# Kernel optimization log

Hardware: AMD Instinct MI355X
Metric: run time of the kernel (lower is better)

The kernel has to match this reference:

```python
import jax, jax.numpy as jnp
import numpy as np

TAU = 0.11
ALPHA = 32.0  # scale
EPS = 1e-12   # torch F.normalize eps


def _l2norm(t):
    n = jnp.linalg.norm(t, axis=-1, keepdims=True)
    return t / jnp.maximum(n, EPS)


def setup_inputs() -> dict:
    key = jax.random.key(0)
    k1, k2, k3, k4 = jax.random.split(key, 4)
    B, N, C, D = 8192, 100000, 1000, 768
    return {
        "x": jax.random.normal(k1, (B, D), dtype=jnp.float32),
        "support_features": jax.random.normal(k2, (N, D), dtype=jnp.float32),
        "support_labels": jax.random.randint(k3, (N,), 0, C),
        "W": jax.random.normal(k4, (D, D), dtype=jnp.float32) * 0.02,
        "b": jnp.zeros((D,), dtype=jnp.float32),
        "num_classes": C,
    }


def reference(x, support_features, support_labels, W, b, num_classes):
    def adapter(t):
        h = t @ W.T + b              # nn.Linear(D, D)
        return jax.nn.silu(h) + t    # SiLU + residual (use_zifa)

    embeddings = _l2norm(adapter(x))                      # (B, D)
    support_key = _l2norm(adapter(support_features))      # (N, D)

    # per-class mean prototype via one segment-sum pass
    sums = jax.ops.segment_sum(support_key, support_labels, num_segments=num_classes)  # (C, D)
    counts = jax.ops.segment_sum(
        jnp.ones((support_key.shape[0],), dtype=support_key.dtype),
        support_labels, num_segments=num_classes)          # (C,)
    means = sums / jnp.maximum(counts, 1.0)[:, None]
    prototypes = jnp.where((counts > 0)[:, None], _l2norm(means), 0.0)  # (C, D)

    # mvrec logits: exp(-(alpha - alpha*cos)) / tau
    cos_sim = embeddings @ prototypes.T                    # (B, C)
    logits = jnp.exp(-(ALPHA - ALPHA * cos_sim)) / max(TAU, 1e-9)
    predicts = jax.nn.softmax(logits, axis=-1)
    return predicts, logits, embeddings
```

## Files before the change

### kernel.cpp

```cpp
#include <hip/hip_runtime.h>
#include <hip/hip_bf16.h>
#include <stdint.h>

typedef __bf16 v8bf __attribute__((ext_vector_type(8)));
typedef float  v4f  __attribute__((ext_vector_type(4)));
typedef unsigned short u16;
typedef unsigned int   u32;

#define B_ROWS   8192
#define N_SUP    100000
#define N_CLS    1000
#define DIM      768
#define CPAD     1024
#define MSUP_PAD 100352

__device__ __forceinline__ u16 f2bf(float f) {
    union { float f; u32 u; } v; v.f = f;
    u32 r = 0x7FFFu + ((v.u >> 16) & 1u);
    return (u16)((v.u + r) >> 16);
}
__device__ __forceinline__ float bf2f(u16 b) {
    union { u32 u; float f; } v; v.u = ((u32)b) << 16; return v.f;
}
__device__ __forceinline__ void glds16(const void* g, void* l) {
    __builtin_amdgcn_global_load_lds((const __attribute__((address_space(1))) u32*)g,
                                     (__attribute__((address_space(3))) u32*)l, 16, 0, 0);
}

__device__ __forceinline__ float block_sum(float v, float* red) {
    #pragma unroll
    for (int o = 32; o > 0; o >>= 1) v += __shfl_down(v, o);
    int wv = threadIdx.x >> 6, ln = threadIdx.x & 63;
    if (ln == 0) red[wv] = v;
    __syncthreads();
    return red[0] + red[1] + red[2] + red[3];
}
__device__ __forceinline__ float block_max(float v, float* red) {
    #pragma unroll
    for (int o = 32; o > 0; o >>= 1) v = fmaxf(v, __shfl_down(v, o));
    int wv = threadIdx.x >> 6, ln = threadIdx.x & 63;
    if (ln == 0) red[wv] = v;
    __syncthreads();
    return fmaxf(fmaxf(red[0], red[1]), fmaxf(red[2], red[3]));
}

__global__ void conv_pad_kernel(const float* __restrict__ in, u16* __restrict__ out,
                                int n_real) {
    int r = blockIdx.x;
    size_t ob = (size_t)r * DIM + threadIdx.x * 4;
    ushort4 o;
    if (r < n_real) {
        float4 v = *(const float4*)(in + ob);
        o.x = f2bf(v.x); o.y = f2bf(v.y); o.z = f2bf(v.z); o.w = f2bf(v.w);
    } else {
        o.x = 0; o.y = 0; o.z = 0; o.w = 0;
    }
    *(ushort4*)(out + ob) = o;
}

__global__ __launch_bounds__(256)
void adapter_gemm_kernel(const u16* __restrict__ A, const u16* __restrict__ Wb,
                         const float* __restrict__ bias,
                         u16* __restrict__ val, float* __restrict__ ss) {
    __shared__ u16 As[128 * 64];
    __shared__ u16 Bs[128 * 64];

    const int tid  = threadIdx.x;
    const int wave = tid >> 6, lane = tid & 63;
    const int fq = lane >> 4, fr = lane & 15;
    const int blk_m = blockIdx.y * 128, blk_n = blockIdx.x * 128;
    const int wm = (wave & 1) * 64, wn = (wave >> 1) * 64;

    v4f acc[4][4];
    #pragma unroll
    for (int i = 0; i < 4; i++)
        #pragma unroll
        for (int j = 0; j < 4; j++) acc[i][j] = (v4f){0.f, 0.f, 0.f, 0.f};

    const int rb = lane >> 3;
    const int cb = (lane & 7) * 8;
    const u16* gA = A  + (size_t)(blk_m + wave * 8 + rb) * DIM + cb;
    const u16* gB = Wb + (size_t)(blk_n + wave * 8 + rb) * DIM + cb;

    for (int k0 = 0; k0 < DIM; k0 += 64) {
        #pragma unroll
        for (int p = 0; p < 4; p++) {
            glds16(gA + (size_t)p * 32 * DIM + k0, As + p * 2048 + wave * 512);
            glds16(gB + (size_t)p * 32 * DIM + k0, Bs + p * 2048 + wave * 512);
        }
        __syncthreads();
        #pragma unroll
        for (int ks = 0; ks < 2; ks++) {
            const int kk = ks * 32;
            v8bf af[4], bfr[4];
            #pragma unroll
            for (int i = 0; i < 4; i++) {
                af[i]  = *(const v8bf*)(As + (wm + i * 16 + fr) * 64 + kk + fq * 8);
                bfr[i] = *(const v8bf*)(Bs + (wn + i * 16 + fr) * 64 + kk + fq * 8);
            }
            #pragma unroll
            for (int i = 0; i < 4; i++)
                #pragma unroll
                for (int j = 0; j < 4; j++)
                    acc[i][j] = __builtin_amdgcn_mfma_f32_16x16x32_bf16(
                        af[i], bfr[j], acc[i][j], 0, 0, 0);
        }
        __syncthreads();
    }

    #pragma unroll
    for (int i = 0; i < 4; i++) {
        int r0 = blk_m + wm + i * 16 + fq * 4;
        float ssp[4] = {0.f, 0.f, 0.f, 0.f};
        #pragma unroll
        for (int j = 0; j < 4; j++) {
            int col = blk_n + wn + j * 16 + fr;
            float bv = bias[col];
            #pragma unroll
            for (int r2 = 0; r2 < 4; r2++) {
                int gr = r0 + r2;
                float h = acc[i][j][r2] + bv;
                float t = bf2f(A[(size_t)gr * DIM + col]);
                float v = h / (1.f + __expf(-h)) + t;
                ssp[r2] += v * v;
                val[(size_t)gr * DIM + col] = f2bf(v);
            }
        }
        #pragma unroll
        for (int r2 = 0; r2 < 4; r2++) {
            float s = ssp[r2];
            s += __shfl_xor(s, 1); s += __shfl_xor(s, 2);
            s += __shfl_xor(s, 4); s += __shfl_xor(s, 8);
            if (fr == 0) atomicAdd(&ss[r0 + r2], s);
        }
    }
}

__global__ void norm_x_kernel(const u16* __restrict__ val, const float* __restrict__ ss,
                              float* __restrict__ emb, u16* __restrict__ emb_bf) {
    int row = blockIdx.x;
    float sc = 1.f / fmaxf(sqrtf(ss[row]), 1e-12f);
    size_t b = (size_t)row * DIM + threadIdx.x * 4;
    ushort4 v = *(const ushort4*)(val + b);
    float4 o;
    o.x = bf2f(v.x) * sc; o.y = bf2f(v.y) * sc;
    o.z = bf2f(v.z) * sc; o.w = bf2f(v.w) * sc;
    *(float4*)(emb + b) = o;
    ushort4 ob; ob.x = f2bf(o.x); ob.y = f2bf(o.y); ob.z = f2bf(o.z); ob.w = f2bf(o.w);
    *(ushort4*)(emb_bf + b) = ob;
}

__global__ __launch_bounds__(256)
void proto_kernel(const u16* __restrict__ val_bf, const float* __restrict__ ss,
                  const int* __restrict__ labels, u16* __restrict__ proto_bf) {
    __shared__ int queue[256];
    __shared__ int qn;
    __shared__ float red[4];
    const int cls = blockIdx.x, tid = threadIdx.x;
    if (tid == 0) qn = 0;
    __syncthreads();
    for (int i4 = tid; i4 < N_SUP / 4; i4 += 256) {
        int4 L = *(const int4*)(labels + i4 * 4);
        if (L.x == cls) queue[atomicAdd(&qn, 1) & 255] = i4 * 4;
        if (L.y == cls) queue[atomicAdd(&qn, 1) & 255] = i4 * 4 + 1;
        if (L.z == cls) queue[atomicAdd(&qn, 1) & 255] = i4 * 4 + 2;
        if (L.w == cls) queue[atomicAdd(&qn, 1) & 255] = i4 * 4 + 3;
    }
    __syncthreads();
    const int n = qn < 256 ? qn : 256;
    float a0 = 0.f, a1 = 0.f, a2 = 0.f;
    for (int e = 0; e < n; e++) {
        int row = queue[e];
        float sc = 1.f / fmaxf(sqrtf(ss[row]), 1e-12f);
        const u16* vr = val_bf + (size_t)row * DIM;
        a0 += bf2f(vr[tid])       * sc;
        a1 += bf2f(vr[tid + 256]) * sc;
        a2 += bf2f(vr[tid + 512]) * sc;
    }
    float inv_cnt = 1.f / fmaxf((float)n, 1.f);
    float m0 = a0 * inv_cnt, m1 = a1 * inv_cnt, m2 = a2 * inv_cnt;
    float tot = block_sum(m0 * m0 + m1 * m1 + m2 * m2, red);
    float sc2 = (n > 0) ? 1.f / fmaxf(sqrtf(tot), 1e-12f) : 0.f;
    size_t b = (size_t)cls * DIM;
    proto_bf[b + tid]       = f2bf(m0 * sc2);
    proto_bf[b + tid + 256] = f2bf(m1 * sc2);
    proto_bf[b + tid + 512] = f2bf(m2 * sc2);
}

__global__ __launch_bounds__(256)
void cos_gemm_kernel(const u16* __restrict__ Ab, const u16* __restrict__ Pb,
                     float* __restrict__ logits) {
    __shared__ u16 As[128 * 64];
    __shared__ u16 Bs[128 * 64];
    const int tid  = threadIdx.x;
    const int wave = tid >> 6, lane = tid & 63;
    const int fq = lane >> 4, fr = lane & 15;
    const int blk_m = blockIdx.y * 128, blk_n = blockIdx.x * 128;
    const int wm = (wave & 1) * 64, wn = (wave >> 1) * 64;

    v4f acc[4][4];
    #pragma unroll
    for (int i = 0; i < 4; i++)
        #pragma unroll
        for (int j = 0; j < 4; j++) acc[i][j] = (v4f){0.f, 0.f, 0.f, 0.f};

    const int rb = lane >> 3;
    const int cb = (lane & 7) * 8;
    const u16* gA = Ab + (size_t)(blk_m + wave * 8 + rb) * DIM + cb;
    const u16* gB = Pb + (size_t)(blk_n + wave * 8 + rb) * DIM + cb;

    for (int k0 = 0; k0 < DIM; k0 += 64) {
        #pragma unroll
        for (int p = 0; p < 4; p++) {
            glds16(gA + (size_t)p * 32 * DIM + k0, As + p * 2048 + wave * 512);
            glds16(gB + (size_t)p * 32 * DIM + k0, Bs + p * 2048 + wave * 512);
        }
        __syncthreads();
        #pragma unroll
        for (int ks = 0; ks < 2; ks++) {
            const int kk = ks * 32;
            v8bf af[4], bfr[4];
            #pragma unroll
            for (int i = 0; i < 4; i++) {
                af[i]  = *(const v8bf*)(As + (wm + i * 16 + fr) * 64 + kk + fq * 8);
                bfr[i] = *(const v8bf*)(Bs + (wn + i * 16 + fr) * 64 + kk + fq * 8);
            }
            #pragma unroll
            for (int i = 0; i < 4; i++)
                #pragma unroll
                for (int j = 0; j < 4; j++)
                    acc[i][j] = __builtin_amdgcn_mfma_f32_16x16x32_bf16(
                        af[i], bfr[j], acc[i][j], 0, 0, 0);
        }
        __syncthreads();
    }

    #pragma unroll
    for (int i = 0; i < 4; i++) {
        int r0 = blk_m + wm + i * 16 + fq * 4;
        #pragma unroll
        for (int j = 0; j < 4; j++) {
            int col = blk_n + wn + j * 16 + fr;
            if (col < N_CLS) {
                #pragma unroll
                for (int r2 = 0; r2 < 4; r2++) {
                    float c = acc[i][j][r2];
                    logits[(size_t)(r0 + r2) * N_CLS + col] =
                        __expf(32.0f * (c - 1.0f)) * (1.0f / 0.11f);
                }
            }
        }
    }
}

__global__ __launch_bounds__(256)
void softmax_kernel(const float* __restrict__ logits, float* __restrict__ predicts) {
    __shared__ float redm[4];
    __shared__ float reds[4];
    int row = blockIdx.x, tid = threadIdx.x;
    const float* lr = logits + (size_t)row * N_CLS;
    float4 lg = make_float4(-1.f, -1.f, -1.f, -1.f);
    bool act = tid < N_CLS / 4;
    if (act) lg = *(const float4*)(lr + tid * 4);
    float mx = fmaxf(fmaxf(lg.x, lg.y), fmaxf(lg.z, lg.w));
    float mxt = block_max(mx, redm);
    float4 e = make_float4(0.f, 0.f, 0.f, 0.f);
    float s = 0.f;
    if (act) {
        e.x = __expf(lg.x - mxt); e.y = __expf(lg.y - mxt);
        e.z = __expf(lg.z - mxt); e.w = __expf(lg.w - mxt);
        s = e.x + e.y + e.z + e.w;
    }
    float st = block_sum(s, reds);
    float inv = 1.f / st;
    if (act) {
        float4 o; o.x = e.x * inv; o.y = e.y * inv; o.z = e.z * inv; o.w = e.w * inv;
        *(float4*)(predicts + (size_t)row * N_CLS + tid * 4) = o;
    }
}

extern "C" void kernel_launch(void* const* d_in, const int* in_sizes, int n_in,
                              void* d_out, int out_size, void* d_ws, size_t ws_size,
                              hipStream_t stream) {
    const float* x      = (const float*)d_in[0];
    const float* sup    = (const float*)d_in[1];
    const int*   labels = (const int*)d_in[2];
    const float* W      = (const float*)d_in[3];
    const float* bias   = (const float*)d_in[4];

    float* predicts = (float*)d_out;
    float* logits   = predicts + (size_t)B_ROWS * N_CLS;
    float* emb      = logits + (size_t)B_ROWS * N_CLS;

    char* ws = (char*)d_ws;
    size_t off = 0;
    u16*   w_bf     = (u16*)(ws + off);   off += (size_t)DIM * DIM * 2;
    u16*   x_bf     = (u16*)(ws + off);   off += (size_t)B_ROWS * DIM * 2;
    u16*   sup_bf   = (u16*)(ws + off);   off += (size_t)MSUP_PAD * DIM * 2;
    u16*   val_x    = (u16*)(ws + off);   off += (size_t)B_ROWS * DIM * 2;
    u16*   val_sup  = (u16*)(ws + off);   off += (size_t)MSUP_PAD * DIM * 2;
    u16*   emb_bf   = (u16*)(ws + off);   off += (size_t)B_ROWS * DIM * 2;
    u16*   proto_bf = (u16*)(ws + off);   off += (size_t)CPAD * DIM * 2;
    float* ss_sup   = (float*)(ws + off); off += (size_t)MSUP_PAD * 4;
    float* ss_x     = (float*)(ws + off); off += (size_t)B_ROWS * 4;

    hipMemsetAsync(ss_sup, 0, ((size_t)MSUP_PAD + B_ROWS) * 4, stream);

    conv_pad_kernel<<<DIM,      192, 0, stream>>>(W,   w_bf,   DIM);
    conv_pad_kernel<<<B_ROWS,   192, 0, stream>>>(x,   x_bf,   B_ROWS);
    conv_pad_kernel<<<MSUP_PAD, 192, 0, stream>>>(sup, sup_bf, N_SUP);

    adapter_gemm_kernel<<<dim3(DIM / 128, B_ROWS / 128), 256, 0, stream>>>(
        x_bf, w_bf, bias, val_x, ss_x);
    adapter_gemm_kernel<<<dim3(DIM / 128, MSUP_PAD / 128), 256, 0, stream>>>(
        sup_bf, w_bf, bias, val_sup, ss_sup);

    norm_x_kernel<<<B_ROWS, 192, 0, stream>>>(val_x, ss_x, emb, emb_bf);

    proto_kernel<<<CPAD, 256, 0, stream>>>(val_sup, ss_sup, labels, proto_bf);

    cos_gemm_kernel<<<dim3(CPAD / 128, B_ROWS / 128), 256, 0, stream>>>(
        emb_bf, proto_bf, logits);
    softmax_kernel<<<B_ROWS, 256, 0, stream>>>(logits, predicts);
}
```

Baseline: 912.0 us.

## Double-buffer GEMM LDS loads, add XCD tile swizzle, widen conversion blocks

Both GEMM kernels now use two LDS buffers, so the next K-slice is loaded asynchronously while the current one feeds the MFMAs. Block IDs are remapped with an XCD-aware swizzle so neighbouring tiles run on the same XCD and share L2. The fp32-to-bf16 conversion kernel now processes four rows per 256-thread block instead of one row per 192-thread block. Costs are doubled LDS per block, which may lower occupancy, and the swizzle assumes the tile count divides evenly by 8.

Result: no change. 907.9 us (-0.4%).

```diff
diff --git a/kernel.cpp b/kernel.cpp
--- a/kernel.cpp
+++ b/kernel.cpp
@@ -10,8 +10,8 @@
 #define B_ROWS   8192
 #define N_SUP    100000
 #define N_CLS    1000
+#define CPAD     1024
 #define DIM      768
-#define CPAD     1024
 #define MSUP_PAD 100352
 
 __device__ __forceinline__ u16 f2bf(float f) {
@@ -44,31 +44,47 @@
     return fmaxf(fmaxf(red[0], red[1]), fmaxf(red[2], red[3]));
 }
 
-__global__ void conv_pad_kernel(const float* __restrict__ in, u16* __restrict__ out,
-                                int n_real) {
-    int r = blockIdx.x;
-    size_t ob = (size_t)r * DIM + threadIdx.x * 4;
-    ushort4 o;
-    if (r < n_real) {
-        float4 v = *(const float4*)(in + ob);
-        o.x = f2bf(v.x); o.y = f2bf(v.y); o.z = f2bf(v.z); o.w = f2bf(v.w);
-    } else {
-        o.x = 0; o.y = 0; o.z = 0; o.w = 0;
-    }
-    *(ushort4*)(out + ob) = o;
+__device__ __forceinline__ int xcd_swizzle(void) {
+    const int nwg = gridDim.x * gridDim.y;
+    const int bid = blockIdx.y * gridDim.x + blockIdx.x;
+    const int q = nwg >> 3;
+    return (bid & 7) * q + (bid >> 3);
+}
+
+__global__ __launch_bounds__(256)
+void conv_pad_kernel(const float* __restrict__ in, u16* __restrict__ out,
+                     int n_real) {
+    #pragma unroll
+    for (int s = 0; s < 3; s++) {
+        size_t f4 = (size_t)blockIdx.x * 768 + s * 256 + threadIdx.x;
+        int row = (int)(f4 / 192);
+        size_t eb = f4 * 4;
+        ushort4 o;
+        if (row < n_real) {
+            float4 v = *(const float4*)(in + eb);
+            o.x = f2bf(v.x); o.y = f2bf(v.y); o.z = f2bf(v.z); o.w = f2bf(v.w);
+        } else {
+            o.x = 0; o.y = 0; o.z = 0; o.w = 0;
+        }
+        *(ushort4*)(out + eb) = o;
+    }
 }
 
 __global__ __launch_bounds__(256)
 void adapter_gemm_kernel(const u16* __restrict__ A, const u16* __restrict__ Wb,
                          const float* __restrict__ bias,
                          u16* __restrict__ val, float* __restrict__ ss) {
-    __shared__ u16 As[128 * 64];
-    __shared__ u16 Bs[128 * 64];
+    __shared__ u16 As[2][128 * 64];
+    __shared__ u16 Bs[2][128 * 64];
 
     const int tid  = threadIdx.x;
     const int wave = tid >> 6, lane = tid & 63;
     const int fq = lane >> 4, fr = lane & 15;
-    const int blk_m = blockIdx.y * 128, blk_n = blockIdx.x * 128;
+
+    const int swz = xcd_swizzle();
+    const int blk_m = (swz / gridDim.x) * 128;
+    const int blk_n = (swz % gridDim.x) * 128;
+
     const int wm = (wave & 1) * 64, wn = (wave >> 1) * 64;
 
     v4f acc[4][4];
@@ -82,21 +98,22 @@
     const u16* gA = A  + (size_t)(blk_m + wave * 8 + rb) * DIM + cb;
     const u16* gB = Wb + (size_t)(blk_n + wave * 8 + rb) * DIM + cb;
 
-    for (int k0 = 0; k0 < DIM; k0 += 64) {
+    auto STAGE = [&](int buf, int k0) {
         #pragma unroll
         for (int p = 0; p < 4; p++) {
-            glds16(gA + (size_t)p * 32 * DIM + k0, As + p * 2048 + wave * 512);
-            glds16(gB + (size_t)p * 32 * DIM + k0, Bs + p * 2048 + wave * 512);
-        }
-        __syncthreads();
+            glds16(gA + (size_t)p * 32 * DIM + k0, &As[buf][p * 2048 + wave * 512]);
+            glds16(gB + (size_t)p * 32 * DIM + k0, &Bs[buf][p * 2048 + wave * 512]);
+        }
+    };
+    auto COMPUTE = [&](int buf) {
         #pragma unroll
         for (int ks = 0; ks < 2; ks++) {
             const int kk = ks * 32;
             v8bf af[4], bfr[4];
             #pragma unroll
             for (int i = 0; i < 4; i++) {
-                af[i]  = *(const v8bf*)(As + (wm + i * 16 + fr) * 64 + kk + fq * 8);
-                bfr[i] = *(const v8bf*)(Bs + (wn + i * 16 + fr) * 64 + kk + fq * 8);
+                af[i]  = *(const v8bf*)(&As[buf][(wm + i * 16 + fr) * 64 + kk + fq * 8]);
+                bfr[i] = *(const v8bf*)(&Bs[buf][(wn + i * 16 + fr) * 64 + kk + fq * 8]);
             }
             #pragma unroll
             for (int i = 0; i < 4; i++)
@@ -105,8 +122,18 @@
                     acc[i][j] = __builtin_amdgcn_mfma_f32_16x16x32_bf16(
                         af[i], bfr[j], acc[i][j], 0, 0, 0);
         }
+    };
+
+    STAGE(0, 0);
+    __syncthreads();
+    int cur = 0;
+    for (int k0 = 64; k0 < DIM; k0 += 64) {
+        STAGE(cur ^ 1, k0);
+        COMPUTE(cur);
         __syncthreads();
-    }
+        cur ^= 1;
+    }
+    COMPUTE(cur);
 
     #pragma unroll
     for (int i = 0; i < 4; i++) {
@@ -190,12 +217,16 @@
 __global__ __launch_bounds__(256)
 void cos_gemm_kernel(const u16* __restrict__ Ab, const u16* __restrict__ Pb,
                      float* __restrict__ logits) {
-    __shared__ u16 As[128 * 64];
-    __shared__ u16 Bs[128 * 64];
+    __shared__ u16 As[2][128 * 64];
+    __shared__ u16 Bs[2][128 * 64];
     const int tid  = threadIdx.x;
     const int wave = tid >> 6, lane = tid & 63;
     const int fq = lane >> 4, fr = lane & 15;
-    const int blk_m = blockIdx.y * 128, blk_n = blockIdx.x * 128;
+
+    const int swz = xcd_swizzle();
+    const int blk_m = (swz / gridDim.x) * 128;
+    const int blk_n = (swz % gridDim.x) * 128;
+
     const int wm = (wave & 1) * 64, wn = (wave >> 1) * 64;
 
     v4f acc[4][4];
@@ -209,21 +240,22 @@
     const u16* gA = Ab + (size_t)(blk_m + wave * 8 + rb) * DIM + cb;
     const u16* gB = Pb + (size_t)(blk_n + wave * 8 + rb) * DIM + cb;
 
-    for (int k0 = 0; k0 < DIM; k0 += 64) {
+    auto STAGE = [&](int buf, int k0) {
         #pragma unroll
         for (int p = 0; p < 4; p++) {
-            glds16(gA + (size_t)p * 32 * DIM + k0, As + p * 2048 + wave * 512);
-            glds16(gB + (size_t)p * 32 * DIM + k0, Bs + p * 2048 + wave * 512);
-        }
-        __syncthreads();
+            glds16(gA + (size_t)p * 32 * DIM + k0, &As[buf][p * 2048 + wave * 512]);
+            glds16(gB + (size_t)p * 32 * DIM + k0, &Bs[buf][p * 2048 + wave * 512]);
+        }
+    };
+    auto COMPUTE = [&](int buf) {
         #pragma unroll
         for (int ks = 0; ks < 2; ks++) {
             const int kk = ks * 32;
             v8bf af[4], bfr[4];
             #pragma unroll
             for (int i = 0; i < 4; i++) {
-                af[i]  = *(const v8bf*)(As + (wm + i * 16 + fr) * 64 + kk + fq * 8);
-                bfr[i] = *(const v8bf*)(Bs + (wn + i * 16 + fr) * 64 + kk + fq * 8);
+                af[i]  = *(const v8bf*)(&As[buf][(wm + i * 16 + fr) * 64 + kk + fq * 8]);
+                bfr[i] = *(const v8bf*)(&Bs[buf][(wn + i * 16 + fr) * 64 + kk + fq * 8]);
             }
             #pragma unroll
             for (int i = 0; i < 4; i++)
@@ -232,8 +264,18 @@
                     acc[i][j] = __builtin_amdgcn_mfma_f32_16x16x32_bf16(
                         af[i], bfr[j], acc[i][j], 0, 0, 0);
         }
+    };
+
+    STAGE(0, 0);
+    __syncthreads();
+    int cur = 0;
+    for (int k0 = 64; k0 < DIM; k0 += 64) {
+        STAGE(cur ^ 1, k0);
+        COMPUTE(cur);
         __syncthreads();
-    }
+        cur ^= 1;
+    }
+    COMPUTE(cur);
 
     #pragma unroll
     for (int i = 0; i < 4; i++) {
@@ -306,9 +348,9 @@
 
     hipMemsetAsync(ss_sup, 0, ((size_t)MSUP_PAD + B_ROWS) * 4, stream);
 
-    conv_pad_kernel<<<DIM,      192, 0, stream>>>(W,   w_bf,   DIM);
-    conv_pad_kernel<<<B_ROWS,   192, 0, stream>>>(x,   x_bf,   B_ROWS);
-    conv_pad_kernel<<<MSUP_PAD, 192, 0, stream>>>(sup, sup_bf, N_SUP);
+    conv_pad_kernel<<<DIM / 4,      256, 0, stream>>>(W,   w_bf,   DIM);
+    conv_pad_kernel<<<B_ROWS / 4,   256, 0, stream>>>(x,   x_bf,   B_ROWS);
+    conv_pad_kernel<<<MSUP_PAD / 4, 256, 0, stream>>>(sup, sup_bf, N_SUP);
 
     adapter_gemm_kernel<<<dim3(DIM / 128, B_ROWS / 128), 256, 0, stream>>>(
         x_bf, w_bf, bias, val_x, ss_x);
```
